# Optimization experiments

Hardware: AMD Instinct MI355X
Metric: run time of the kernel (lower is better)

## Reference

```python
import jax, jax.numpy as jnp
import numpy as np


def setup_inputs() -> dict:
    key = jax.random.key(0)
    features = jax.random.normal(key, (8192, 512), dtype=jnp.float32)
    return {"features": features}


def reference(features):
    # Pairwise L2 distance via the GEMM trick (avoids the N x N x D broadcast
    # intermediate the original torch code materializes):
    #   ||a - b||^2 = ||a||^2 + ||b||^2 - 2 a.b
    sq_norms = jnp.sum(features * features, axis=-1)            # [N]
    gram = features @ features.T                                # [N, N]
    sq_dist = sq_norms[:, None] + sq_norms[None, :] - 2.0 * gram
    sq_dist = jnp.maximum(sq_dist, 0.0)                         # clamp fp noise
    return -jnp.sqrt(sq_dist)                                   # [N, N]
```

## Files before the change

kernel.cpp:

```cpp
#include <hip/hip_runtime.h>
#include <hip/hip_bf16.h>
#include <math.h>

#define N_ROWS 8192
#define DIM    512

typedef __bf16 bf16x8 __attribute__((ext_vector_type(8)));
typedef float  floatx4 __attribute__((ext_vector_type(4)));

__device__ __forceinline__ unsigned short f2bf_rne(float x) {
    union { float f; unsigned u; } v; v.f = x;
    unsigned r = v.u + 0x7FFFu + ((v.u >> 16) & 1u);
    return (unsigned short)(r >> 16);
}

__device__ __forceinline__ void async_cp16(const void* g, void* l) {
    __builtin_amdgcn_global_load_lds(
        (const __attribute__((address_space(1))) unsigned int*)g,
        (__attribute__((address_space(3))) unsigned int*)l,
        16, 0, 0);
}

__global__ __launch_bounds__(256) void fs_norm_convert(
    const float* __restrict__ F, unsigned short* __restrict__ Fb,
    float* __restrict__ sn) {
    const int wave = threadIdx.x >> 6;
    const int lane = threadIdx.x & 63;
    const int row  = blockIdx.x * 4 + wave;

    const float4* src = reinterpret_cast<const float4*>(F + (size_t)row * DIM) + lane * 2;
    float4 x0 = src[0];
    float4 x1 = src[1];

    float ss = x0.x*x0.x + x0.y*x0.y + x0.z*x0.z + x0.w*x0.w
             + x1.x*x1.x + x1.y*x1.y + x1.z*x1.z + x1.w*x1.w;

    uint4 p;
    p.x = (unsigned)f2bf_rne(x0.x) | ((unsigned)f2bf_rne(x0.y) << 16);
    p.y = (unsigned)f2bf_rne(x0.z) | ((unsigned)f2bf_rne(x0.w) << 16);
    p.z = (unsigned)f2bf_rne(x1.x) | ((unsigned)f2bf_rne(x1.y) << 16);
    p.w = (unsigned)f2bf_rne(x1.z) | ((unsigned)f2bf_rne(x1.w) << 16);
    reinterpret_cast<uint4*>(Fb + (size_t)row * DIM)[lane] = p;

    #pragma unroll
    for (int off = 32; off > 0; off >>= 1) ss += __shfl_down(ss, off);
    if (lane == 0) sn[row] = ss;
}

__global__ __launch_bounds__(256) void fs_gemm(
    const unsigned short* __restrict__ Fb, const float* __restrict__ sn,
    float* __restrict__ out) {
    __shared__ unsigned short As[128 * 32];
    __shared__ unsigned short Bs[128 * 32];

    const int tid  = threadIdx.x;
    const int lane = tid & 63;
    const int wave = tid >> 6;
    const int wr   = wave >> 1;
    const int wc   = wave & 1;
    const int quad = lane >> 4;
    const int l16  = lane & 15;

    const int bRow = blockIdx.y * 128;
    const int bCol = blockIdx.x * 128;

    floatx4 acc[4][4];
    #pragma unroll
    for (int i = 0; i < 4; ++i)
        #pragma unroll
        for (int j = 0; j < 4; ++j)
            acc[i][j] = floatx4{0.f, 0.f, 0.f, 0.f};

    const int sRow = tid >> 2;
    const int sCol = (tid & 3) * 8;
    const unsigned short* gA = Fb + (size_t)(bRow + sRow) * DIM + sCol;
    const unsigned short* gB = Fb + (size_t)(bCol + sRow) * DIM + sCol;
    const size_t half = (size_t)64 * DIM;

    unsigned short* ldsA = As + tid * 8;
    unsigned short* ldsB = Bs + tid * 8;

    for (int k0 = 0; k0 < DIM; k0 += 32) {
        async_cp16(gA,        ldsA);
        async_cp16(gA + half, ldsA + 2048);
        async_cp16(gB,        ldsB);
        async_cp16(gB + half, ldsB + 2048);
        gA += 32; gB += 32;
        __syncthreads();

        bf16x8 af[4], bf[4];
        #pragma unroll
        for (int t = 0; t < 4; ++t) {
            af[t] = *reinterpret_cast<const bf16x8*>(
                As + ((wr * 64 + t * 16 + l16) * 32 + quad * 8));
            bf[t] = *reinterpret_cast<const bf16x8*>(
                Bs + ((wc * 64 + t * 16 + l16) * 32 + quad * 8));
        }
        #pragma unroll
        for (int i = 0; i < 4; ++i)
            #pragma unroll
            for (int j = 0; j < 4; ++j)
                acc[i][j] = __builtin_amdgcn_mfma_f32_16x16x32_bf16(
                    af[i], bf[j], acc[i][j], 0, 0, 0);
        __syncthreads();
    }

    const int row0 = bRow + wr * 64;
    const int col0 = bCol + wc * 64;
    float snc[4];
    #pragma unroll
    for (int j = 0; j < 4; ++j) snc[j] = sn[col0 + j * 16 + l16];

    #pragma unroll
    for (int i = 0; i < 4; ++i) {
        #pragma unroll
        for (int r = 0; r < 4; ++r) {
            const int row = row0 + i * 16 + quad * 4 + r;
            const float snr = sn[row];
            float* orow = out + (size_t)row * N_ROWS;
            #pragma unroll
            for (int j = 0; j < 4; ++j) {
                const int col = col0 + j * 16 + l16;
                float v = snr + snc[j] - 2.0f * acc[i][j][r];
                v = fmaxf(v, 0.0f);
                orow[col] = (row == col) ? 0.0f : -sqrtf(v);
            }
        }
    }
}

extern "C" void kernel_launch(void* const* d_in, const int* in_sizes, int n_in,
                              void* d_out, int out_size, void* d_ws, size_t ws_size,
                              hipStream_t stream) {
    const float* F = (const float*)d_in[0];
    float* out = (float*)d_out;

    unsigned short* Fb = (unsigned short*)d_ws;
    float* sn = (float*)((char*)d_ws + (size_t)N_ROWS * DIM * 2);

    fs_norm_convert<<<N_ROWS / 4, 256, 0, stream>>>(F, Fb, sn);

    dim3 grid(N_ROWS / 128, N_ROWS / 128);
    fs_gemm<<<grid, 256, 0, stream>>>(Fb, sn, out);
}
```

Measured before the change: 350.7 us.

## Exploit distance-matrix symmetry with triangular tiles, double-buffered swizzled LDS

The GEMM now launches only lower-triangular 128x128 tiles. Each off-diagonal block computes both the tile and its transpose by issuing a second MFMA with swapped operands, then writes both output tiles. This halves global and LDS operand traffic per output tile, but MFMA work per output element is unchanged. The K loop moves to 64-wide steps with a double buffer so the next stage loads while the current one computes, uses an XOR-swizzled LDS layout to avoid bank conflicts, and interleaves the block index across eight groups. Costs are doubled accumulator registers, handled with launch_bounds(256,2), and an uneven workload between diagonal and off-diagonal blocks.

```diff
diff --git a/kernel.cpp b/kernel.cpp
--- a/kernel.cpp
+++ b/kernel.cpp
@@ -1,9 +1,10 @@
 #include <hip/hip_runtime.h>
-#include <hip/hip_bf16.h>
 #include <math.h>
 
 #define N_ROWS 8192
 #define DIM    512
+#define NT     (N_ROWS / 128)
+#define NBLK   (NT * (NT + 1) / 2)
 
 typedef __bf16 bf16x8 __attribute__((ext_vector_type(8)));
 typedef float  floatx4 __attribute__((ext_vector_type(4)));
@@ -47,11 +48,11 @@
     if (lane == 0) sn[row] = ss;
 }
 
-__global__ __launch_bounds__(256) void fs_gemm(
+__global__ __launch_bounds__(256, 2) void fs_gemm_sym(
     const unsigned short* __restrict__ Fb, const float* __restrict__ sn,
     float* __restrict__ out) {
-    __shared__ unsigned short As[128 * 32];
-    __shared__ unsigned short Bs[128 * 32];
+    __shared__ unsigned short As[2][128 * 64];
+    __shared__ unsigned short Bs[2][128 * 64];
 
     const int tid  = threadIdx.x;
     const int lane = tid & 63;
@@ -61,69 +62,135 @@
     const int quad = lane >> 4;
     const int l16  = lane & 15;
 
-    const int bRow = blockIdx.y * 128;
-    const int bCol = blockIdx.x * 128;
-
-    floatx4 acc[4][4];
+    int L = (int)blockIdx.x;
+    L = (L & 7) * (NBLK / 8) + (L >> 3);
+    int bi = (int)((sqrtf(8.0f * (float)L + 1.0f) - 1.0f) * 0.5f);
+    while ((bi + 1) * (bi + 2) / 2 <= L) ++bi;
+    while (bi * (bi + 1) / 2 > L) --bi;
+    const int bj   = L - bi * (bi + 1) / 2;
+    const int diag = (bi == bj);
+
+    const int bRow = bi * 128;
+    const int bCol = bj * 128;
+
+    floatx4 acc[4][4], accT[4][4];
     #pragma unroll
     for (int i = 0; i < 4; ++i)
         #pragma unroll
-        for (int j = 0; j < 4; ++j)
-            acc[i][j] = floatx4{0.f, 0.f, 0.f, 0.f};
-
-    const int sRow = tid >> 2;
-    const int sCol = (tid & 3) * 8;
-    const unsigned short* gA = Fb + (size_t)(bRow + sRow) * DIM + sCol;
-    const unsigned short* gB = Fb + (size_t)(bCol + sRow) * DIM + sCol;
-    const size_t half = (size_t)64 * DIM;
-
-    unsigned short* ldsA = As + tid * 8;
-    unsigned short* ldsB = Bs + tid * 8;
-
-    for (int k0 = 0; k0 < DIM; k0 += 32) {
-        async_cp16(gA,        ldsA);
-        async_cp16(gA + half, ldsA + 2048);
-        async_cp16(gB,        ldsB);
-        async_cp16(gB + half, ldsB + 2048);
-        gA += 32; gB += 32;
+        for (int j = 0; j < 4; ++j) {
+            acc[i][j]  = floatx4{0.f, 0.f, 0.f, 0.f};
+            accT[i][j] = floatx4{0.f, 0.f, 0.f, 0.f};
+        }
+
+    const int r   = tid >> 3;
+    const int c   = tid & 7;
+    const int csw = c ^ (r & 7);
+    const unsigned short* gA = Fb + (size_t)(bRow + r) * DIM + csw * 8;
+    const unsigned short* gB = Fb + (size_t)(bCol + r) * DIM + csw * 8;
+
+    const int cg0 = ((0 + quad) ^ (l16 & 7)) * 8;
+    const int cg1 = ((4 + quad) ^ (l16 & 7)) * 8;
+
+    #define STAGE(buf, k0) {                                        \
+        unsigned short* la = &As[buf][tid * 8];                     \
+        unsigned short* lb = &Bs[buf][tid * 8];                     \
+        const unsigned short* pa = gA + (k0);                       \
+        const unsigned short* pb = gB + (k0);                       \
+        async_cp16(pa,            la);                              \
+        async_cp16(pa + 32 * DIM, la + 2048);                       \
+        async_cp16(pa + 64 * DIM, la + 4096);                       \
+        async_cp16(pa + 96 * DIM, la + 6144);                       \
+        async_cp16(pb,            lb);                              \
+        async_cp16(pb + 32 * DIM, lb + 2048);                       \
+        async_cp16(pb + 64 * DIM, lb + 4096);                       \
+        async_cp16(pb + 96 * DIM, lb + 6144);                       \
+    }
+
+    STAGE(0, 0)
+    __syncthreads();
+
+    for (int k = 0; k < DIM / 64; ++k) {
+        if (k < DIM / 64 - 1) STAGE((k + 1) & 1, (k + 1) * 64)
+        const unsigned short* Ab = As[k & 1];
+        const unsigned short* Bb = Bs[k & 1];
+        #pragma unroll
+        for (int h = 0; h < 2; ++h) {
+            const int cg = h ? cg1 : cg0;
+            bf16x8 af[4], bf[4];
+            #pragma unroll
+            for (int t = 0; t < 4; ++t) {
+                af[t] = *reinterpret_cast<const bf16x8*>(
+                    Ab + (wr * 64 + t * 16 + l16) * 64 + cg);
+                bf[t] = *reinterpret_cast<const bf16x8*>(
+                    Bb + (wc * 64 + t * 16 + l16) * 64 + cg);
+            }
+            if (diag) {
+                #pragma unroll
+                for (int i = 0; i < 4; ++i)
+                    #pragma unroll
+                    for (int j = 0; j < 4; ++j)
+                        acc[i][j] = __builtin_amdgcn_mfma_f32_16x16x32_bf16(
+                            af[i], bf[j], acc[i][j], 0, 0, 0);
+            } else {
+                #pragma unroll
+                for (int i = 0; i < 4; ++i)
+                    #pragma unroll
+                    for (int j = 0; j < 4; ++j) {
+                        acc[i][j]  = __builtin_amdgcn_mfma_f32_16x16x32_bf16(
+                            af[i], bf[j], acc[i][j], 0, 0, 0);
+                        accT[i][j] = __builtin_amdgcn_mfma_f32_16x16x32_bf16(
+                            bf[i], af[j], accT[i][j], 0, 0, 0);
+                    }
+            }
+        }
         __syncthreads();
-
-        bf16x8 af[4], bf[4];
-        #pragma unroll
-        for (int t = 0; t < 4; ++t) {
-            af[t] = *reinterpret_cast<const bf16x8*>(
-                As + ((wr * 64 + t * 16 + l16) * 32 + quad * 8));
-            bf[t] = *reinterpret_cast<const bf16x8*>(
-                Bs + ((wc * 64 + t * 16 + l16) * 32 + quad * 8));
-        }
-        #pragma unroll
-        for (int i = 0; i < 4; ++i)
+    }
+
+    {
+        const int row0 = bRow + wr * 64;
+        const int col0 = bCol + wc * 64;
+        float snc[4];
+        #pragma unroll
+        for (int j = 0; j < 4; ++j) snc[j] = sn[col0 + j * 16 + l16];
+
+        #pragma unroll
+        for (int i = 0; i < 4; ++i) {
             #pragma unroll
-            for (int j = 0; j < 4; ++j)
-                acc[i][j] = __builtin_amdgcn_mfma_f32_16x16x32_bf16(
-                    af[i], bf[j], acc[i][j], 0, 0, 0);
-        __syncthreads();
-    }
-
-    const int row0 = bRow + wr * 64;
-    const int col0 = bCol + wc * 64;
-    float snc[4];
-    #pragma unroll
-    for (int j = 0; j < 4; ++j) snc[j] = sn[col0 + j * 16 + l16];
-
-    #pragma unroll
-    for (int i = 0; i < 4; ++i) {
-        #pragma unroll
-        for (int r = 0; r < 4; ++r) {
-            const int row = row0 + i * 16 + quad * 4 + r;
-            const float snr = sn[row];
-            float* orow = out + (size_t)row * N_ROWS;
+            for (int rr = 0; rr < 4; ++rr) {
+                const int row = row0 + i * 16 + quad * 4 + rr;
+                const float snr = sn[row];
+                float* orow = out + (size_t)row * N_ROWS;
+                #pragma unroll
+                for (int j = 0; j < 4; ++j) {
+                    const int col = col0 + j * 16 + l16;
+                    float v = snr + snc[j] - 2.0f * acc[i][j][rr];
+                    v = fmaxf(v, 0.0f);
+                    orow[col] = (row == col) ? 0.0f : -sqrtf(v);
+                }
+            }
+        }
+    }
+
+    if (!diag) {
+        const int rowT0 = bCol + wc * 64;
+        const int colT0 = bRow + wr * 64;
+        float snq[4];
+        #pragma unroll
+        for (int q = 0; q < 4; ++q) snq[q] = sn[colT0 + q * 16 + l16];
+
+        #pragma unroll
+        for (int p = 0; p < 4; ++p) {
             #pragma unroll
-            for (int j = 0; j < 4; ++j) {
-                const int col = col0 + j * 16 + l16;
-                float v = snr + snc[j] - 2.0f * acc[i][j][r];
-                v = fmaxf(v, 0.0f);
-                orow[col] = (row == col) ? 0.0f : -sqrtf(v);
+            for (int rr = 0; rr < 4; ++rr) {
+                const int row = rowT0 + p * 16 + quad * 4 + rr;
+                const float snr = sn[row];
+                float* orow = out + (size_t)row * N_ROWS;
+                #pragma unroll
+                for (int q = 0; q < 4; ++q) {
+                    const int col = colT0 + q * 16 + l16;
+                    float v = snr + snq[q] - 2.0f * accT[p][q][rr];
+                    orow[col] = -sqrtf(fmaxf(v, 0.0f));
+                }
             }
         }
     }
@@ -140,6 +207,5 @@
 
     fs_norm_convert<<<N_ROWS / 4, 256, 0, stream>>>(F, Fb, sn);
 
-    dim3 grid(N_ROWS / 128, N_ROWS / 128);
-    fs_gemm<<<grid, 256, 0, stream>>>(Fb, sn, out);
-}
+    fs_gemm_sym<<<dim3(NBLK), 256, 0, stream>>>(Fb, sn, out);
+}
```

After: 503.9 us. 1.44x slower.
